# Performance work log

Measured on AMD Instinct MI355X. Metric: run time of the kernel, lower is better.

Reference implementation:

```python
import jax, jax.numpy as jnp
import numpy as np

B = 65536      # batch
FDIM = 256     # features_dim (flatten extractor => obs dim)
ADIM = 8       # action dim
T = 3          # n_tasks
H = 256        # net_arch width
IN = FDIM + ADIM

_PARAM_SHAPES = [("W1", (T, IN, H)), ("b1", (T, H)), ("W2", (T, H, H)), ("b2", (T, H)),
                 ("W3", (T, H, H)), ("b3", (T, H)), ("W4", (T, H, 1)), ("b4", (T, 1))]

def setup_inputs() -> dict:
    key = jax.random.key(0)
    ks = jax.random.split(key, 2 + 2 * len(_PARAM_SHAPES))
    d = {"obs": jax.random.normal(ks[0], (B, FDIM), dtype=jnp.float32),
         "actions": jax.random.normal(ks[1], (B, ADIM), dtype=jnp.float32)}
    i = 2
    for q in ("q1", "q2"):
        for name, sh in _PARAM_SHAPES:
            d[f"{q}_{name}"] = jax.random.normal(ks[i], sh, dtype=jnp.float32) * 0.05
            i += 1
    return d

def _heads(x, W1, b1, W2, b2, W3, b3, W4, b4):
    # x: [B, IN]; per-task stacked MLP -> [T, B]
    h = jax.nn.relu(jnp.einsum('bi,tih->tbh', x, W1) + b1[:, None, :])
    h = jax.nn.relu(jnp.einsum('tbh,thk->tbk', h, W2) + b2[:, None, :])
    h = jax.nn.relu(jnp.einsum('tbh,thk->tbk', h, W3) + b3[:, None, :])
    return (jnp.einsum('tbh,tho->tbo', h, W4) + b4[:, None, :])[..., 0]

def reference(obs, actions,
              q1_W1, q1_b1, q1_W2, q1_b2, q1_W3, q1_b3, q1_W4, q1_b4,
              q2_W1, q2_b1, q2_W2, q2_b2, q2_W3, q2_b3, q2_W4, q2_b4):
    x = jnp.concatenate([obs, actions], axis=1)           # [B, IN]
    task = jnp.argmax(obs[:, -T:], axis=-1)               # [B] hard top-1 routing
    mask = jax.nn.one_hot(task, T, dtype=x.dtype).T       # [T, B]
    y1 = _heads(x, q1_W1, q1_b1, q1_W2, q1_b2, q1_W3, q1_b3, q1_W4, q1_b4)  # [T, B]
    y2 = _heads(x, q2_W1, q2_b1, q2_W2, q2_b2, q2_W3, q2_b3, q2_W4, q2_b4)
    q1 = jnp.sum(y1 * mask, axis=0)[:, None]              # [B, 1]
    q2 = jnp.sum(y2 * mask, axis=0)[:, None]
    return (q1, q2)
```

## Files before the change

kernel.cpp:

```cpp
#include <hip/hip_runtime.h>
#include <hip/hip_bf16.h>


#define NB 65536
#define MROWS 64
#define XSTR 296
#define HSTR 264

typedef __attribute__((ext_vector_type(8))) short short8;
typedef __attribute__((ext_vector_type(4))) short short4v;
typedef __attribute__((ext_vector_type(4))) float f32x4;

__device__ __forceinline__ float bf2f(unsigned short u){
  union { unsigned int i; float f; } x; x.i = ((unsigned int)u) << 16; return x.f;
}
__device__ __forceinline__ unsigned short f2bf(float f){
  unsigned int x = __float_as_uint(f);
  x += 0x7fffu + ((x >> 16) & 1u);
  return (unsigned short)(x >> 16);
}
__device__ __forceinline__ float ldval(const void* p, int idx, int isbf16){
  return isbf16 ? bf2f(((const unsigned short*)p)[idx]) : ((const float*)p)[idx];
}

__device__ __forceinline__ int block_sniff(const void* obs, int tid, int* sflag){
  if (tid < 64) {
    unsigned short u = ((const unsigned short*)obs)[tid * 2];
    int e = (u >> 7) & 0xFF;
    unsigned long long m = __ballot(e >= 110 && e <= 132);
    if (tid == 0) *sflag = (__popcll(m) >= 32) ? 1 : 0;
  }
  __syncthreads();
  return *sflag;
}

struct KParams {
  const void* obs;
  const void* act;
  const unsigned short* w1t[2];
  const unsigned short* w2t[2];
  const unsigned short* w3t[2];
  const void* b1[2];
  const void* b2[2];
  const void* b3[2];
  const void* w4[2];
  const void* b4[2];
  const int* counts;
  const int* perm;
  void* out;
};

__device__ __forceinline__ int task_of(const void* obs, int b, int isbf16){
  float v0, v1, v2;
  if (isbf16) {
    short4v u = *(const short4v*)((const unsigned short*)obs + b * 256 + 252);
    v0 = bf2f((unsigned short)u[1]); v1 = bf2f((unsigned short)u[2]); v2 = bf2f((unsigned short)u[3]);
  } else {
    f32x4 u = *(const f32x4*)((const float*)obs + b * 256 + 252);
    v0 = u[1]; v1 = u[2]; v2 = u[3];
  }
  int t = 0; float m = v0;
  if (v1 > m) { m = v1; t = 1; }
  if (v2 > m) { t = 2; }
  return t;
}

__global__ void prep_count(const void* q1W1, const void* q1W2, const void* q1W3,
                           const void* q2W1, const void* q2W2, const void* q2W3,
                           const void* obs, unsigned short* out,
                           int* hist, unsigned char* tasks){
  __shared__ int sflag;
  int tid = threadIdx.x;
  int isbf16 = block_sniff(obs, tid, &sflag);
  if (blockIdx.x >= 600) {
    __shared__ int h[3];
    if (tid < 3) h[tid] = 0;
    __syncthreads();
    int blk = blockIdx.x - 600;
    int b = blk * 256 + tid;
    int t = task_of(obs, b, isbf16);
    tasks[b] = (unsigned char)t;
    atomicAdd(&h[t], 1);
    __syncthreads();
    if (tid < 3) hist[blk * 3 + tid] = h[tid];
    return;
  }
  int gid8 = (blockIdx.x * 256 + tid) * 8;
  int net = gid8 / 614400;
  int idx = gid8 - net * 614400;
  const void* W1 = net ? q2W1 : q1W1;
  const void* W2 = net ? q2W2 : q1W2;
  const void* W3 = net ? q2W3 : q1W3;
  short8 sv;
  if (idx < 221184) {
    int t = idx / 73728; int i = idx - t * 73728;
    int g = i / 4608;  int r = i - g * 4608;
    int kb = r >> 9;   int q2 = r & 511;
    int l16 = q2 >> 5; int rem = q2 & 31;
    int n = g * 16 + l16;
    int k = kb * 32 + (rem & ~7);
    #pragma unroll
    for (int j = 0; j < 8; j++) {
      int kk = k + j;
      sv[j] = (kk < 264) ? (short)f2bf(ldval(W1, (t * 264 + kk) * 256 + n, isbf16)) : (short)0;
    }
  } else if (idx < 417792) {
    int j0 = idx - 221184;
    int t = j0 >> 16; int i = j0 & 65535;
    int g = i >> 12;  int r = i & 4095;
    int kb = r >> 9;  int q2 = r & 511;
    int l16 = q2 >> 5; int rem = q2 & 31;
    int n = g * 16 + l16;
    int k = kb * 32 + (rem & ~7);
    #pragma unroll
    for (int j = 0; j < 8; j++)
      sv[j] = (short)f2bf(ldval(W2, t * 65536 + (k + j) * 256 + n, isbf16));
  } else {
    int j0 = idx - 417792;
    int t = j0 >> 16; int i = j0 & 65535;
    int g = i >> 12;  int r = i & 4095;
    int kb = r >> 9;  int q2 = r & 511;
    int l16 = q2 >> 5; int rem = q2 & 31;
    int n = g * 16 + l16;
    int k = kb * 32 + (rem & ~7);
    #pragma unroll
    for (int j = 0; j < 8; j++)
      sv[j] = (short)f2bf(ldval(W3, t * 65536 + (k + j) * 256 + n, isbf16));
  }
  *(short8*)(out + net * 614400 + idx) = sv;
}

__global__ void route_scatter(const unsigned char* __restrict__ tasks,
                              const int* __restrict__ hist,
                              int* counts, int* perm){
  __shared__ int sh[3][256];
  __shared__ int totals[3], pres[3], base[3], zz[3];
  int tid = threadIdx.x;
  int blk = blockIdx.x;
  sh[0][tid] = hist[tid * 3 + 0];
  sh[1][tid] = hist[tid * 3 + 1];
  sh[2][tid] = hist[tid * 3 + 2];
  if (tid < 3) zz[tid] = 0;
  __syncthreads();
  if (tid < 3) {
    int tot = 0, pre = 0;
    for (int b = 0; b < 256; b++) {
      int v = sh[tid][b];
      if (b < blk) pre += v;
      tot += v;
    }
    totals[tid] = tot; pres[tid] = pre;
  }
  __syncthreads();
  if (tid < 3) {
    int a0 = ((totals[0] + MROWS - 1) / MROWS) * MROWS;
    int a1 = ((totals[1] + MROWS - 1) / MROWS) * MROWS;
    int off = (tid == 0) ? 0 : (tid == 1) ? a0 : a0 + a1;
    base[tid] = off + pres[tid];
    if (blk == 0) counts[tid] = totals[tid];
  }
  __syncthreads();
  int b = blk * 256 + tid;
  int t = tasks[b];
  int r = atomicAdd(&zz[t], 1);
  perm[base[t] + r] = b;
}

template<int KC> struct BF { short8 v[KC][2]; };

template<int KC>
__device__ __forceinline__ void load_bf(BF<KC>& f, const unsigned short* __restrict__ wt,
                                        int wave, int quad, int l16){
  const unsigned short* wg = wt + (wave * 2) * (KC * 512) + l16 * 32 + quad * 8;
  #pragma unroll
  for (int kb = 0; kb < KC; ++kb) {
    f.v[kb][0] = *(const short8*)(wg + kb * 512);
    f.v[kb][1] = *(const short8*)(wg + KC * 512 + kb * 512);
  }
}

template<int KC>
__device__ __forceinline__ void mfma_layer(const unsigned short* __restrict__ lin, int lstride,
                                           const BF<KC>& f, f32x4 acc[4][2],
                                           int quad, int l16){
  const f32x4 z = {0.f, 0.f, 0.f, 0.f};
  #pragma unroll
  for (int kb = 0; kb < KC; ++kb) {
    short8 afr[4];
    int ko = kb * 32 + quad * 8;
    #pragma unroll
    for (int mt = 0; mt < 4; mt++)
      afr[mt] = *(const short8*)(lin + (mt * 16 + l16) * lstride + ko);
    #pragma unroll
    for (int mt = 0; mt < 4; mt++)
      #pragma unroll
      for (int nt = 0; nt < 2; nt++)
        acc[mt][nt] = __builtin_amdgcn_mfma_f32_16x16x32_bf16(
            afr[mt], f.v[kb][nt], (kb == 0) ? z : acc[mt][nt], 0, 0, 0);
  }
}

__device__ __forceinline__ void epilogue(f32x4 acc[4][2], float bv0, float bv1,
                                         unsigned short* lout, int quad, int l16, int nbase){
  #pragma unroll
  for (int mt = 0; mt < 4; mt++)
    #pragma unroll
    for (int nt = 0; nt < 2; nt++) {
      float bv = nt ? bv1 : bv0;
      f32x4 a = acc[mt][nt];
      #pragma unroll
      for (int r = 0; r < 4; r++) {
        float v = fmaxf(a[r] + bv, 0.f);
        lout[(mt * 16 + quad * 4 + r) * HSTR + nbase + nt * 16 + l16] = f2bf(v);
      }
    }
}

__global__ __launch_bounds__(512, 4) void fused_kernel(KParams p){
  __shared__ unsigned short X[MROWS * XSTR];
  __shared__ unsigned short HA[MROWS * HSTR];
  unsigned short* HB = X;
  int* sflag = (int*)HA;

  int tid = threadIdx.x;
  int net = blockIdx.y;
  int p0  = blockIdx.x * MROWS;
  int wave = tid >> 6, lane = tid & 63, quad = lane >> 4, l16 = lane & 15;
  int nbase = wave * 32;

  int c0 = p.counts[0], c1 = p.counts[1], c2 = p.counts[2];
  int off1 = ((c0 + MROWS - 1) / MROWS) * MROWS;
  int off2 = off1 + ((c1 + MROWS - 1) / MROWS) * MROWS;
  int task  = (p0 >= off2) ? 2 : ((p0 >= off1) ? 1 : 0);
  int segend = (task == 0) ? c0 : (task == 1) ? off1 + c1 : off2 + c2;

  BF<9> f1;
  load_bf<9>(f1, p.w1t[net] + task * 73728, wave, quad, l16);

  int isbf16 = block_sniff(p.obs, tid, sflag);
  int bsz = isbf16 ? 2 : 4;

  {
    int srow = tid >> 3, seg = tid & 7;
    int pos = p0 + srow;
    int r = (pos < segend) ? p.perm[pos] : -1;
    #pragma unroll
    for (int j = 0; j < 5; ++j) {
      int c = seg + 8 * j;
      if (c <= 35) {
        short8 sv = {0,0,0,0,0,0,0,0};
        if (r >= 0 && c < 33) {
          if (isbf16) {
            const unsigned short* src = (c < 32) ? ((const unsigned short*)p.obs + r * 256 + c * 8)
                                                 : ((const unsigned short*)p.act + r * 8);
            sv = *(const short8*)src;
          } else {
            const float* src = (c < 32) ? ((const float*)p.obs + r * 256 + c * 8)
                                        : ((const float*)p.act + r * 8);
            f32x4 a = *(const f32x4*)src;
            f32x4 b = *(const f32x4*)(src + 4);
            #pragma unroll
            for (int q = 0; q < 4; q++) { sv[q] = (short)f2bf(a[q]); sv[4 + q] = (short)f2bf(b[q]); }
          }
        }
        *(short8*)(X + srow * XSTR + c * 8) = sv;
      }
    }
  }
  __syncthreads();

  f32x4 acc[4][2];

  const char* b1p = (const char*)p.b1[net] + task * 256 * bsz;
  float bva0 = ldval(b1p, nbase + l16, isbf16);
  float bva1 = ldval(b1p, nbase + 16 + l16, isbf16);
  mfma_layer<9>(X, XSTR, f1, acc, quad, l16);
  BF<8> f2;
  load_bf<8>(f2, p.w2t[net] + task * 65536, wave, quad, l16);
  epilogue(acc, bva0, bva1, HA, quad, l16, nbase);
  __syncthreads();

  const char* b2p = (const char*)p.b2[net] + task * 256 * bsz;
  float bvb0 = ldval(b2p, nbase + l16, isbf16);
  float bvb1 = ldval(b2p, nbase + 16 + l16, isbf16);
  mfma_layer<8>(HA, HSTR, f2, acc, quad, l16);
  BF<8> f3;
  load_bf<8>(f3, p.w3t[net] + task * 65536, wave, quad, l16);
  epilogue(acc, bvb0, bvb1, HB, quad, l16, nbase);
  __syncthreads();

  const char* b3p = (const char*)p.b3[net] + task * 256 * bsz;
  float bvc0 = ldval(b3p, nbase + l16, isbf16);
  float bvc1 = ldval(b3p, nbase + 16 + l16, isbf16);
  mfma_layer<8>(HB, HSTR, f3, acc, quad, l16);

  int seg = tid & 7, row = tid >> 3;
  float wv[32];
  if (isbf16) {
    const unsigned short* w4p = (const unsigned short*)p.w4[net] + task * 256 + seg * 32;
    #pragma unroll
    for (int q = 0; q < 4; q++) {
      short8 t = *(const short8*)(w4p + q * 8);
      #pragma unroll
      for (int j = 0; j < 8; j++) wv[q * 8 + j] = bf2f((unsigned short)t[j]);
    }
  } else {
    const float* w4p = (const float*)p.w4[net] + task * 256 + seg * 32;
    #pragma unroll
    for (int q = 0; q < 8; q++) {
      f32x4 a = *(const f32x4*)(w4p + q * 4);
      #pragma unroll
      for (int j = 0; j < 4; j++) wv[q * 4 + j] = a[j];
    }
  }
  float b4v = ldval(p.b4[net], task, isbf16);
  epilogue(acc, bvc0, bvc1, HA, quad, l16, nbase);
  __syncthreads();

  {
    float s = 0.f;
    #pragma unroll
    for (int kk = 0; kk < 32; kk += 8) {
      short8 hv = *(const short8*)(HA + row * HSTR + seg * 32 + kk);
      #pragma unroll
      for (int j = 0; j < 8; j++)
        s += bf2f((unsigned short)hv[j]) * wv[kk + j];
    }
    s += __shfl_xor(s, 1);
    s += __shfl_xor(s, 2);
    s += __shfl_xor(s, 4);
    if (seg == 0) {
      int pos = p0 + row;
      if (pos < segend) {
        int r = p.perm[pos];
        float y = s + b4v;
        if (isbf16) ((unsigned short*)p.out)[net * NB + r] = f2bf(y);
        else        ((float*)p.out)[net * NB + r] = y;
      }
    }
  }
}

extern "C" void kernel_launch(void* const* d_in, const int* in_sizes, int n_in,
                              void* d_out, int out_size, void* d_ws, size_t ws_size,
                              hipStream_t stream) {
  char* ws = (char*)d_ws;
  int* counts  = (int*)ws;
  int* hist    = (int*)(ws + 64);
  unsigned char* tasks = (unsigned char*)(ws + 3200);
  int* perm    = (int*)(ws + 68800);
  unsigned short* wts  = (unsigned short*)(ws + 331520);

  const void* obs = d_in[0];
  const void* act = d_in[1];

  prep_count<<<856, 256, 0, stream>>>(d_in[2], d_in[4], d_in[6],
                                      d_in[10], d_in[12], d_in[14],
                                      obs, wts, hist, tasks);
  route_scatter<<<256, 256, 0, stream>>>(tasks, hist, counts, perm);

  KParams kp;
  kp.obs = obs; kp.act = act;
  for (int q = 0; q < 2; q++) {
    int base = 2 + q * 8;
    kp.b1[q] = d_in[base + 1];
    kp.b2[q] = d_in[base + 3];
    kp.b3[q] = d_in[base + 5];
    kp.w4[q] = d_in[base + 6];
    kp.b4[q] = d_in[base + 7];
    kp.w1t[q] = wts + q * 614400;
    kp.w2t[q] = wts + q * 614400 + 221184;
    kp.w3t[q] = wts + q * 614400 + 417792;
  }
  kp.counts = counts; kp.perm = perm;
  kp.out = d_out;

  fused_kernel<<<dim3(1026, 2), 512, 0, stream>>>(kp);
}
```

Before: 215.0 us.

## Transpose MFMA roles: stream weights as A operand with prefetch, split waves 4x2

Each layer is restructured so the weights become the MFMA A operand and the activations the B operand. Waves are tiled 4x2 over the hidden and row dimensions, and each wave streams weight fragments from global memory with a one-step prefetch instead of preloading all of them into registers. Epilogue stores now pack outputs into 64-bit writes, and the block-wide dtype sniff becomes a per-wave ballot, which drops one __syncthreads and a shared flag. This is meant to lower register pressure for the target of 4 blocks per CU and to cut scalar LDS stores. In exchange, weight loads now sit in the inner k loop, so each block rereads weights through cache and global latency may be exposed.

Result: slower. 262.8 us (+22.2%).

```diff
diff --git a/kernel.cpp b/kernel.cpp
--- a/kernel.cpp
+++ b/kernel.cpp
@@ -10,6 +10,7 @@
 typedef __attribute__((ext_vector_type(8))) short short8;
 typedef __attribute__((ext_vector_type(4))) short short4v;
 typedef __attribute__((ext_vector_type(4))) float f32x4;
+typedef __attribute__((ext_vector_type(2))) unsigned int uint2v;
 
 __device__ __forceinline__ float bf2f(unsigned short u){
   union { unsigned int i; float f; } x; x.i = ((unsigned int)u) << 16; return x.f;
@@ -23,15 +24,11 @@
   return isbf16 ? bf2f(((const unsigned short*)p)[idx]) : ((const float*)p)[idx];
 }
 
-__device__ __forceinline__ int block_sniff(const void* obs, int tid, int* sflag){
-  if (tid < 64) {
-    unsigned short u = ((const unsigned short*)obs)[tid * 2];
-    int e = (u >> 7) & 0xFF;
-    unsigned long long m = __ballot(e >= 110 && e <= 132);
-    if (tid == 0) *sflag = (__popcll(m) >= 32) ? 1 : 0;
-  }
-  __syncthreads();
-  return *sflag;
+__device__ __forceinline__ int wave_sniff(const void* obs, int lane){
+  unsigned short u = ((const unsigned short*)obs)[lane * 2];
+  int e = (u >> 7) & 0xFF;
+  unsigned long long m = __ballot(e >= 110 && e <= 132);
+  return (__popcll(m) >= 32) ? 1 : 0;
 }
 
 struct KParams {
@@ -69,9 +66,8 @@
                            const void* q2W1, const void* q2W2, const void* q2W3,
                            const void* obs, unsigned short* out,
                            int* hist, unsigned char* tasks){
-  __shared__ int sflag;
   int tid = threadIdx.x;
-  int isbf16 = block_sniff(obs, tid, &sflag);
+  int isbf16 = wave_sniff(obs, tid & 63);
   if (blockIdx.x >= 600) {
     __shared__ int h[3];
     if (tid < 3) h[tid] = 0;
@@ -166,67 +162,76 @@
   perm[base[t] + r] = b;
 }
 
-template<int KC> struct BF { short8 v[KC][2]; };
-
 template<int KC>
-__device__ __forceinline__ void load_bf(BF<KC>& f, const unsigned short* __restrict__ wt,
-                                        int wave, int quad, int l16){
-  const unsigned short* wg = wt + (wave * 2) * (KC * 512) + l16 * 32 + quad * 8;
+__device__ __forceinline__ void run_layer_T(const unsigned short* __restrict__ lin, int lstride,
+                                            const unsigned short* __restrict__ wt,
+                                            const void* bias, unsigned short* __restrict__ lout,
+                                            int isbf16, int mg, int ng, int quad, int l16){
+  float bv[4][4];
+  #pragma unroll
+  for (int tm = 0; tm < 4; tm++) {
+    int hb = mg * 64 + tm * 16 + quad * 4;
+    #pragma unroll
+    for (int r = 0; r < 4; r++) bv[tm][r] = ldval(bias, hb + r, isbf16);
+  }
+  const unsigned short* wg[4];
+  #pragma unroll
+  for (int tm = 0; tm < 4; tm++)
+    wg[tm] = wt + (mg * 4 + tm) * (KC * 512) + l16 * 32 + quad * 8;
+
+  short8 a[4], an[4];
+  #pragma unroll
+  for (int tm = 0; tm < 4; tm++) a[tm] = *(const short8*)(wg[tm]);
+
+  f32x4 acc[4][2];
+  const f32x4 z = {0.f, 0.f, 0.f, 0.f};
   #pragma unroll
   for (int kb = 0; kb < KC; ++kb) {
-    f.v[kb][0] = *(const short8*)(wg + kb * 512);
-    f.v[kb][1] = *(const short8*)(wg + KC * 512 + kb * 512);
-  }
-}
-
-template<int KC>
-__device__ __forceinline__ void mfma_layer(const unsigned short* __restrict__ lin, int lstride,
-                                           const BF<KC>& f, f32x4 acc[4][2],
-                                           int quad, int l16){
-  const f32x4 z = {0.f, 0.f, 0.f, 0.f};
-  #pragma unroll
-  for (int kb = 0; kb < KC; ++kb) {
-    short8 afr[4];
-    int ko = kb * 32 + quad * 8;
-    #pragma unroll
-    for (int mt = 0; mt < 4; mt++)
-      afr[mt] = *(const short8*)(lin + (mt * 16 + l16) * lstride + ko);
-    #pragma unroll
-    for (int mt = 0; mt < 4; mt++)
-      #pragma unroll
-      for (int nt = 0; nt < 2; nt++)
-        acc[mt][nt] = __builtin_amdgcn_mfma_f32_16x16x32_bf16(
-            afr[mt], f.v[kb][nt], (kb == 0) ? z : acc[mt][nt], 0, 0, 0);
-  }
-}
-
-__device__ __forceinline__ void epilogue(f32x4 acc[4][2], float bv0, float bv1,
-                                         unsigned short* lout, int quad, int l16, int nbase){
-  #pragma unroll
-  for (int mt = 0; mt < 4; mt++)
-    #pragma unroll
-    for (int nt = 0; nt < 2; nt++) {
-      float bv = nt ? bv1 : bv0;
-      f32x4 a = acc[mt][nt];
-      #pragma unroll
-      for (int r = 0; r < 4; r++) {
-        float v = fmaxf(a[r] + bv, 0.f);
-        lout[(mt * 16 + quad * 4 + r) * HSTR + nbase + nt * 16 + l16] = f2bf(v);
-      }
-    }
+    if (kb + 1 < KC) {
+      #pragma unroll
+      for (int tm = 0; tm < 4; tm++)
+        an[tm] = *(const short8*)(wg[tm] + (kb + 1) * 512);
+    }
+    short8 bfr[2];
+    #pragma unroll
+    for (int tn = 0; tn < 2; tn++)
+      bfr[tn] = *(const short8*)(lin + (ng * 32 + tn * 16 + l16) * lstride + kb * 32 + quad * 8);
+    #pragma unroll
+    for (int tm = 0; tm < 4; tm++)
+      #pragma unroll
+      for (int tn = 0; tn < 2; tn++)
+        acc[tm][tn] = __builtin_amdgcn_mfma_f32_16x16x32_bf16(
+            a[tm], bfr[tn], (kb == 0) ? z : acc[tm][tn], 0, 0, 0);
+    if (kb + 1 < KC) {
+      #pragma unroll
+      for (int tm = 0; tm < 4; tm++) a[tm] = an[tm];
+    }
+  }
+  #pragma unroll
+  for (int tm = 0; tm < 4; tm++) {
+    #pragma unroll
+    for (int tn = 0; tn < 2; tn++) {
+      f32x4 v = acc[tm][tn];
+      unsigned int u0 = (unsigned int)f2bf(fmaxf(v[0] + bv[tm][0], 0.f))
+                      | ((unsigned int)f2bf(fmaxf(v[1] + bv[tm][1], 0.f)) << 16);
+      unsigned int u1 = (unsigned int)f2bf(fmaxf(v[2] + bv[tm][2], 0.f))
+                      | ((unsigned int)f2bf(fmaxf(v[3] + bv[tm][3], 0.f)) << 16);
+      uint2v w; w[0] = u0; w[1] = u1;
+      *(uint2v*)(lout + (ng * 32 + tn * 16 + l16) * HSTR + mg * 64 + tm * 16 + quad * 4) = w;
+    }
+  }
 }
 
 __global__ __launch_bounds__(512, 4) void fused_kernel(KParams p){
   __shared__ unsigned short X[MROWS * XSTR];
   __shared__ unsigned short HA[MROWS * HSTR];
   unsigned short* HB = X;
-  int* sflag = (int*)HA;
 
   int tid = threadIdx.x;
   int net = blockIdx.y;
   int p0  = blockIdx.x * MROWS;
   int wave = tid >> 6, lane = tid & 63, quad = lane >> 4, l16 = lane & 15;
-  int nbase = wave * 32;
+  int mg = wave & 3, ng = wave >> 2;
 
   int c0 = p.counts[0], c1 = p.counts[1], c2 = p.counts[2];
   int off1 = ((c0 + MROWS - 1) / MROWS) * MROWS;
@@ -234,10 +239,7 @@
   int task  = (p0 >= off2) ? 2 : ((p0 >= off1) ? 1 : 0);
   int segend = (task == 0) ? c0 : (task == 1) ? off1 + c1 : off2 + c2;
 
-  BF<9> f1;
-  load_bf<9>(f1, p.w1t[net] + task * 73728, wave, quad, l16);
-
-  int isbf16 = block_sniff(p.obs, tid, sflag);
+  int isbf16 = wave_sniff(p.obs, lane);
   int bsz = isbf16 ? 2 : 4;
 
   {
@@ -269,30 +271,19 @@
   }
   __syncthreads();
 
-  f32x4 acc[4][2];
-
-  const char* b1p = (const char*)p.b1[net] + task * 256 * bsz;
-  float bva0 = ldval(b1p, nbase + l16, isbf16);
-  float bva1 = ldval(b1p, nbase + 16 + l16, isbf16);
-  mfma_layer<9>(X, XSTR, f1, acc, quad, l16);
-  BF<8> f2;
-  load_bf<8>(f2, p.w2t[net] + task * 65536, wave, quad, l16);
-  epilogue(acc, bva0, bva1, HA, quad, l16, nbase);
-  __syncthreads();
-
-  const char* b2p = (const char*)p.b2[net] + task * 256 * bsz;
-  float bvb0 = ldval(b2p, nbase + l16, isbf16);
-  float bvb1 = ldval(b2p, nbase + 16 + l16, isbf16);
-  mfma_layer<8>(HA, HSTR, f2, acc, quad, l16);
-  BF<8> f3;
-  load_bf<8>(f3, p.w3t[net] + task * 65536, wave, quad, l16);
-  epilogue(acc, bvb0, bvb1, HB, quad, l16, nbase);
-  __syncthreads();
-
-  const char* b3p = (const char*)p.b3[net] + task * 256 * bsz;
-  float bvc0 = ldval(b3p, nbase + l16, isbf16);
-  float bvc1 = ldval(b3p, nbase + 16 + l16, isbf16);
-  mfma_layer<8>(HB, HSTR, f3, acc, quad, l16);
+  run_layer_T<9>(X, XSTR, p.w1t[net] + task * 73728,
+                 (const char*)p.b1[net] + task * 256 * bsz, HA,
+                 isbf16, mg, ng, quad, l16);
+  __syncthreads();
+
+  run_layer_T<8>(HA, HSTR, p.w2t[net] + task * 65536,
+                 (const char*)p.b2[net] + task * 256 * bsz, HB,
+                 isbf16, mg, ng, quad, l16);
+  __syncthreads();
+
+  run_layer_T<8>(HB, HSTR, p.w3t[net] + task * 65536,
+                 (const char*)p.b3[net] + task * 256 * bsz, HA,
+                 isbf16, mg, ng, quad, l16);
 
   int seg = tid & 7, row = tid >> 3;
   float wv[32];
@@ -314,7 +305,6 @@
     }
   }
   float b4v = ldval(p.b4[net], task, isbf16);
-  epilogue(acc, bvc0, bvc1, HA, quad, l16, nbase);
   __syncthreads();
 
   {
```
